# Performance work log

Hardware: AMD Instinct MI355X
Metric: run time of the kernel (lower is better)

## Reference

```python
import jax, jax.numpy as jnp
import numpy as np

SPAN_W = 8      # fixed span width (tokens per span)
HID = 150       # Score hidden dim (hardcoded in source)


def _score_mlp(x, w1, b1, w2, b2, w3, b3):
    # Linear->ReLU->(Dropout=id)->Linear->ReLU->(Dropout=id)->Linear ; out dim 1
    h = jax.nn.relu(x @ w1 + b1)
    h = jax.nn.relu(h @ w2 + b2)
    return h @ w3 + b3


def _make_mlp_params(key, in_dim):
    ks = jax.random.split(key, 6)
    s1 = 1.0 / np.sqrt(in_dim)
    s2 = 1.0 / np.sqrt(HID)
    return (
        jax.random.uniform(ks[0], (in_dim, HID), jnp.float32, -s1, s1),
        jax.random.uniform(ks[1], (HID,), jnp.float32, -s1, s1),
        jax.random.uniform(ks[2], (HID, HID), jnp.float32, -s2, s2),
        jax.random.uniform(ks[3], (HID,), jnp.float32, -s2, s2),
        jax.random.uniform(ks[4], (HID, 1), jnp.float32, -s2, s2),
        jax.random.uniform(ks[5], (1,), jnp.float32, -s2, s2),
    )


def setup_inputs() -> dict:
    key = jax.random.key(0)
    k_emb, k_sp, k_a, k_m, k_p = jax.random.split(key, 5)
    E = 768
    B, T, S = 2, 2048, 96
    encoded_docs = jax.random.normal(k_emb, (B, T, E), jnp.float32)
    span_starts = jnp.sort(
        jax.random.randint(k_sp, (B, S), 0, 2040, dtype=jnp.int64), axis=-1)
    aw1, ab1, aw2, ab2, aw3, ab3 = _make_mlp_params(k_a, E)          # attn Score
    mw1, mb1, mw2, mb2, mw3, mb3 = _make_mlp_params(k_m, 3 * E)      # mention Score
    pw1, pb1, pw2, pb2, pw3, pb3 = _make_mlp_params(k_p, 9 * E)      # pair Score
    return {
        "encoded_docs": encoded_docs, "span_starts": span_starts,
        "aw1": aw1, "ab1": ab1, "aw2": aw2, "ab2": ab2, "aw3": aw3, "ab3": ab3,
        "mw1": mw1, "mb1": mb1, "mw2": mw2, "mb2": mb2, "mw3": mw3, "mb3": mb3,
        "pw1": pw1, "pb1": pb1, "pw2": pw2, "pb2": pb2, "pw3": pw3, "pb3": pb3,
    }


def reference(encoded_docs, span_starts,
              aw1, ab1, aw2, ab2, aw3, ab3,
              mw1, mb1, mw2, mb2, mw3, mb3,
              pw1, pb1, pw2, pb2, pw3, pb3):
    B, T, E = encoded_docs.shape
    S = span_starts.shape[1]

    # --- MentionScore ---
    attns = _score_mlp(encoded_docs, aw1, ab1, aw2, ab2, aw3, ab3)  # [B,T,1]
    starts = span_starts                                              # [B,S]
    ends = starts + (SPAN_W - 1)
    g_start = jnp.take_along_axis(encoded_docs, starts[:, :, None], axis=1)  # [B,S,E]
    g_end = jnp.take_along_axis(encoded_docs, ends[:, :, None], axis=1)      # [B,S,E]
    tok_idx = starts[:, :, None] + jnp.arange(SPAN_W, dtype=starts.dtype)     # [B,S,W]
    flat = tok_idx.reshape(B, S * SPAN_W)
    span_emb = jnp.take_along_axis(encoded_docs, flat[:, :, None], axis=1).reshape(B, S, SPAN_W, E)
    span_attn = jnp.take_along_axis(attns, flat[:, :, None], axis=1).reshape(B, S, SPAN_W, 1)
    g_attn = jnp.sum(span_emb * span_attn, axis=2)                    # [B,S,E]
    g_i = jnp.concatenate([g_start, g_end, g_attn], axis=-1)          # [B,S,3E]
    mention_scores = _score_mlp(g_i, mw1, mb1, mw2, mb2, mw3, mb3)    # [B,S,1]

    # --- PairwiseScore: all pairs (i=span_1, j=span_2) ---
    gi = jnp.broadcast_to(g_i[:, :, None, :], (B, S, S, 3 * E))
    gj = jnp.broadcast_to(g_i[:, None, :, :], (B, S, S, 3 * E))
    pair = jnp.concatenate([gi, gj, gi * gj], axis=-1)                # [B,S,S,9E]
    pair_scores = _score_mlp(pair, pw1, pb1, pw2, pb2, pw3, pb3)      # [B,S,S,1]
    ext = (mention_scores[:, :, None, :] + mention_scores[:, None, :, :] + pair_scores) / 3.0
    return jnp.clip(ext, 0.0, 1.0)
```

## Files before the change

### kernel.cpp

```cpp
#include <hip/hip_runtime.h>

#define EDIM   768
#define E3     2304
#define HIDD   150
#define TT     2048
#define SS     96
#define BB     2

typedef unsigned short u16;
using frag   = __attribute__((ext_vector_type(8))) short;
using f32x4v = __attribute__((ext_vector_type(4))) float;
using u16x8  = __attribute__((ext_vector_type(8))) unsigned short;

__device__ __forceinline__ u16 bf16rn(float f) {
    union { float f; unsigned u; } v; v.f = f;
    unsigned r = v.u + 0x7FFF + ((v.u >> 16) & 1);
    return (u16)(r >> 16);
}
__device__ __forceinline__ float bf16tof(u16 h) {
    union { unsigned u; float f; } v; v.u = ((unsigned)h) << 16;
    return v.f;
}
__device__ __forceinline__ void split2(float f, u16& hi, u16& lo) {
    hi = bf16rn(f); lo = bf16rn(f - bf16tof(hi));
}
__device__ __forceinline__ int swzoff(int row, int qd) {
    return row * 32 + (((qd + (row >> 1)) & 3) << 3);
}
__device__ __forceinline__ void async16(const void* g, void* l) {
    __builtin_amdgcn_global_load_lds(
        (const __attribute__((address_space(1))) void*)g,
        (__attribute__((address_space(3))) void*)l, 16, 0, 0);
}

__global__ __launch_bounds__(256) void k_prep_all(
    const float* __restrict__ pw1, const float* __restrict__ mw1,
    const float* __restrict__ aw1, const float* __restrict__ aw2,
    const float* __restrict__ pw2,
    u16* __restrict__ W12t_hi, u16* __restrict__ W12t_lo,
    u16* __restrict__ AW1t_hi, u16* __restrict__ AW1t_lo,
    u16* __restrict__ AW2t_hi, u16* __restrict__ AW2t_lo,
    u16* __restrict__ PW2t_hi, u16* __restrict__ PW2t_lo)
{
    __shared__ float tile[64][33];
    const int bi = blockIdx.x;
    const int t  = threadIdx.x;

    if (bi < 720) {
        const int k0 = (bi % 36) * 64;
        const int n0 = (bi / 36) * 32;
        const int seg = n0 / 160;
        const int nloc0 = n0 - seg * 160;
        for (int idx = t; idx < 2048; idx += 256) {
            const int kk = idx >> 5, nn = idx & 31;
            const int nl = nloc0 + nn;
            const int k  = k0 + kk;
            float v = 0.f;
            if (nl < HIDD) {
                if (seg == 0)      v = pw1[(long)k * HIDD + nl];
                else if (seg == 1) v = pw1[(long)(E3 + k) * HIDD + nl];
                else if (seg == 2) v = mw1[(long)k * HIDD + nl];
                else               v = pw1[(long)(2 * E3 + k) * HIDD + nl];
            }
            tile[kk][nn] = v;
        }
        __syncthreads();
        for (int idx = t; idx < 2048; idx += 256) {
            const int nn = idx >> 6, kk = idx & 63;
            u16 hi, lo; split2(tile[kk][nn], hi, lo);
            W12t_hi[(long)(n0 + nn) * E3 + k0 + kk] = hi;
            W12t_lo[(long)(n0 + nn) * E3 + k0 + kk] = lo;
        }
    } else if (bi < 1488) {
        const int k = bi - 720;
        if (t < 160) {
            float v = (t < HIDD) ? aw1[k * HIDD + t] : 0.f;
            u16 hi, lo; split2(v, hi, lo);
            AW1t_hi[(long)t * EDIM + k] = hi;
            AW1t_lo[(long)t * EDIM + k] = lo;
        }
    } else {
        const int r = bi - 1488;
        const int k = r % 160;
        const int which = r / 160;
        const float* src = which ? pw2 : aw2;
        u16* dh = which ? PW2t_hi : AW2t_hi;
        u16* dl = which ? PW2t_lo : AW2t_lo;
        if (t < 160) {
            float v = (t < HIDD && k < HIDD) ? src[k * HIDD + t] : 0.f;
            u16 hi, lo; split2(v, hi, lo);
            dh[t * 160 + k] = hi;
            dl[t * 160 + k] = lo;
        }
    }
}

__global__ __launch_bounds__(256) void k_attn1(
    const float* __restrict__ X, const int* __restrict__ spans,
    const u16* __restrict__ AW1t_hi, const u16* __restrict__ AW1t_lo,
    float* __restrict__ AH1)
{
    __shared__ __align__(16) u16 As_hi[32 * 40];
    __shared__ __align__(16) u16 As_lo[32 * 40];
    __shared__ __align__(16) u16 Bs_hi[160 * 40];
    __shared__ __align__(16) u16 Bs_lo[160 * 40];

    const int t    = threadIdx.x;
    const int lane = t & 63;
    const int m    = lane & 15;
    const int quad = lane >> 4;
    const int w    = t >> 6;
    const int mt   = (w & 1) * 16;
    const int nb   = (w >> 1) * 80;
    const int ks   = blockIdx.y;

    const int rr = t >> 3, q = t & 7;
    const int grow = blockIdx.x * 32 + rr;
    const int bs = grow >> 3, sw = grow & 7;
    const int b  = bs / SS;
    const int tok = spans[bs] + sw;
    const float* arow = X + ((long)b * TT + tok) * EDIM;

    f32x4v acc[5];
    #pragma unroll
    for (int ht = 0; ht < 5; ++ht)
        #pragma unroll
        for (int r = 0; r < 4; ++r) acc[ht][r] = 0.f;

    for (int tt = 0; tt < 6; ++tt) {
        const int kk0 = ks * 192 + tt * 32;
        {
            const float4 xv = *(const float4*)&arow[kk0 + q * 4];
            ushort4 hv, lv;
            split2(xv.x, hv.x, lv.x); split2(xv.y, hv.y, lv.y);
            split2(xv.z, hv.z, lv.z); split2(xv.w, hv.w, lv.w);
            *(ushort4*)&As_hi[rr * 40 + q * 4] = hv;
            *(ushort4*)&As_lo[rr * 40 + q * 4] = lv;
        }
        #pragma unroll
        for (int it = 0; it < 3; ++it) {
            const int v = t + it * 256;
            if (v < 640) {
                const int h = v >> 2, qq = v & 3;
                *(uint4*)&Bs_hi[h * 40 + qq * 8] = *(const uint4*)&AW1t_hi[(long)h * EDIM + kk0 + qq * 8];
                *(uint4*)&Bs_lo[h * 40 + qq * 8] = *(const uint4*)&AW1t_lo[(long)h * EDIM + kk0 + qq * 8];
            }
        }
        __syncthreads();
        const frag ah = *(const frag*)&As_hi[(mt + m) * 40 + quad * 8];
        const frag al = *(const frag*)&As_lo[(mt + m) * 40 + quad * 8];
        #pragma unroll
        for (int ht = 0; ht < 5; ++ht) {
            const frag bh = *(const frag*)&Bs_hi[(nb + ht * 16 + m) * 40 + quad * 8];
            const frag bl = *(const frag*)&Bs_lo[(nb + ht * 16 + m) * 40 + quad * 8];
            acc[ht] = __builtin_amdgcn_mfma_f32_16x16x32_bf16(al, bh, acc[ht], 0, 0, 0);
            acc[ht] = __builtin_amdgcn_mfma_f32_16x16x32_bf16(ah, bl, acc[ht], 0, 0, 0);
            acc[ht] = __builtin_amdgcn_mfma_f32_16x16x32_bf16(ah, bh, acc[ht], 0, 0, 0);
        }
        __syncthreads();
    }
    #pragma unroll
    for (int ht = 0; ht < 5; ++ht) {
        #pragma unroll
        for (int r = 0; r < 4; ++r) {
            const int row = blockIdx.x * 32 + mt + quad * 4 + r;
            const int col = nb + ht * 16 + m;
            if (col < HIDD) atomicAdd(&AH1[row * 160 + col], acc[ht][r]);
        }
    }
}

__global__ __launch_bounds__(256) void k_attn2(
    const float* __restrict__ AH1,
    const u16* __restrict__ AW2t_hi, const u16* __restrict__ AW2t_lo,
    const float* __restrict__ ab1, const float* __restrict__ ab2,
    const float* __restrict__ aw3, const float* __restrict__ ab3,
    float* __restrict__ attn_g)
{
    __shared__ __align__(16) u16 As_hi[32 * 40];
    __shared__ __align__(16) u16 As_lo[32 * 40];
    __shared__ __align__(16) u16 Bs_hi[160 * 40];
    __shared__ __align__(16) u16 Bs_lo[160 * 40];
    __shared__ float h1s[32 * 160];
    __shared__ float red[32];

    const int t    = threadIdx.x;
    const int lane = t & 63;
    const int m    = lane & 15;
    const int quad = lane >> 4;
    const int w    = t >> 6;
    const int mt   = (w & 1) * 16;
    const int nb   = (w >> 1) * 80;

    for (int u = t; u < 1280; u += 256) {
        const int row = u / 40, c4 = u - (u / 40) * 40;
        const int c0 = c4 * 4;
        const float4 v = *(const float4*)&AH1[(blockIdx.x * 32 + row) * 160 + c0];
        h1s[row * 160 + c0 + 0] = (c0 + 0 < HIDD) ? fmaxf(v.x + ab1[c0 + 0], 0.f) : 0.f;
        h1s[row * 160 + c0 + 1] = (c0 + 1 < HIDD) ? fmaxf(v.y + ab1[c0 + 1], 0.f) : 0.f;
        h1s[row * 160 + c0 + 2] = (c0 + 2 < HIDD) ? fmaxf(v.z + ab1[c0 + 2], 0.f) : 0.f;
        h1s[row * 160 + c0 + 3] = (c0 + 3 < HIDD) ? fmaxf(v.w + ab1[c0 + 3], 0.f) : 0.f;
    }
    if (t < 32) red[t] = 0.f;
    __syncthreads();

    const int rr = t >> 3, q = t & 7;
    f32x4v acc2[5];
    #pragma unroll
    for (int ht = 0; ht < 5; ++ht)
        #pragma unroll
        for (int r = 0; r < 4; ++r) acc2[ht][r] = 0.f;

    for (int kk = 0; kk < 5; ++kk) {
        {
            const float4 xv = *(const float4*)&h1s[rr * 160 + kk * 32 + q * 4];
            ushort4 hv, lv;
            split2(xv.x, hv.x, lv.x); split2(xv.y, hv.y, lv.y);
            split2(xv.z, hv.z, lv.z); split2(xv.w, hv.w, lv.w);
            *(ushort4*)&As_hi[rr * 40 + q * 4] = hv;
            *(ushort4*)&As_lo[rr * 40 + q * 4] = lv;
        }
        #pragma unroll
        for (int it = 0; it < 3; ++it) {
            const int v = t + it * 256;
            if (v < 640) {
                const int h = v >> 2, qq = v & 3;
                *(uint4*)&Bs_hi[h * 40 + qq * 8] = *(const uint4*)&AW2t_hi[h * 160 + kk * 32 + qq * 8];
                *(uint4*)&Bs_lo[h * 40 + qq * 8] = *(const uint4*)&AW2t_lo[h * 160 + kk * 32 + qq * 8];
            }
        }
        __syncthreads();
        const frag ah = *(const frag*)&As_hi[(mt + m) * 40 + quad * 8];
        const frag al = *(const frag*)&As_lo[(mt + m) * 40 + quad * 8];
        #pragma unroll
        for (int ht = 0; ht < 5; ++ht) {
            const frag bh = *(const frag*)&Bs_hi[(nb + ht * 16 + m) * 40 + quad * 8];
            const frag bl = *(const frag*)&Bs_lo[(nb + ht * 16 + m) * 40 + quad * 8];
            acc2[ht] = __builtin_amdgcn_mfma_f32_16x16x32_bf16(al, bh, acc2[ht], 0, 0, 0);
            acc2[ht] = __builtin_amdgcn_mfma_f32_16x16x32_bf16(ah, bl, acc2[ht], 0, 0, 0);
            acc2[ht] = __builtin_amdgcn_mfma_f32_16x16x32_bf16(ah, bh, acc2[ht], 0, 0, 0);
        }
        __syncthreads();
    }

    float s[4] = {0.f, 0.f, 0.f, 0.f};
    #pragma unroll
    for (int ht = 0; ht < 5; ++ht) {
        const int col = nb + ht * 16 + m;
        if (col < HIDD) {
            const float w3 = aw3[col];
            #pragma unroll
            for (int r = 0; r < 4; ++r)
                s[r] += fmaxf(acc2[ht][r] + ab2[col], 0.f) * w3;
        }
    }
    #pragma unroll
    for (int r = 0; r < 4; ++r) {
        for (int off = 8; off > 0; off >>= 1) s[r] += __shfl_down(s[r], off, 16);
    }
    if (m == 0) {
        #pragma unroll
        for (int r = 0; r < 4; ++r) atomicAdd(&red[mt + quad * 4 + r], s[r]);
    }
    __syncthreads();
    if (t < 32) attn_g[blockIdx.x * 32 + t] = red[t] + ab3[0];
}

__global__ __launch_bounds__(256) void k_span_g(
    const float* __restrict__ X, const int* __restrict__ spans,
    const float* __restrict__ attn_g, float* __restrict__ G_ws,
    u16* __restrict__ Gs_hi, u16* __restrict__ Gs_lo)
{
    __shared__ float a8[8];
    const int t  = threadIdx.x;
    const int bs = blockIdx.x;
    const int b  = bs / SS;
    const int start = spans[bs];
    const float* xb = X + ((long)b * TT + start) * EDIM;
    float* Gp = G_ws + (long)bs * E3;
    u16* Gh = Gs_hi + (long)bs * E3;
    u16* Gl = Gs_lo + (long)bs * E3;
    if (t < 8) a8[t] = attn_g[bs * 8 + t];
    __syncthreads();

    for (int e = t; e < EDIM; e += 256) {
        const float gs = xb[e];
        const float ge = xb[7 * EDIM + e];
        float ga = 0.f;
        #pragma unroll
        for (int w = 0; w < 8; ++w) ga += xb[w * EDIM + e] * a8[w];
        Gp[e] = gs; Gp[EDIM + e] = ge; Gp[2 * EDIM + e] = ga;
        u16 hi, lo;
        split2(gs, hi, lo); Gh[e] = hi;            Gl[e] = lo;
        split2(ge, hi, lo); Gh[EDIM + e] = hi;     Gl[EDIM + e] = lo;
        split2(ga, hi, lo); Gh[2 * EDIM + e] = hi; Gl[2 * EDIM + e] = lo;
    }
}

__global__ __launch_bounds__(256) void k_uvm(
    const u16* __restrict__ Gs_hi, const u16* __restrict__ Gs_lo,
    const u16* __restrict__ W9t_hi, const u16* __restrict__ W9t_lo,
    float* __restrict__ UVM)
{
    __shared__ __align__(16) u16 As_hi[64 * 40];
    __shared__ __align__(16) u16 As_lo[64 * 40];
    __shared__ __align__(16) u16 Bs_hi[160 * 40];
    __shared__ __align__(16) u16 Bs_lo[160 * 40];

    const int t    = threadIdx.x;
    const int mb   = blockIdx.x;
    const int nb   = blockIdx.y;
    const int ks   = blockIdx.z;
    const int lane = t & 63;
    const int m    = lane & 15;
    const int quad = lane >> 4;
    const int w    = t >> 6;
    const int mhalf = (w & 1) * 32;
    const int nbase = (w >> 1) * 80;
    const int arr = t >> 2, aq = t & 3;

    f32x4v acc[2][5];
    #pragma unroll
    for (int i = 0; i < 2; ++i)
        #pragma unroll
        for (int j = 0; j < 5; ++j)
            #pragma unroll
            for (int r = 0; r < 4; ++r) acc[i][j][r] = 0.f;

    for (int tt = 0; tt < 6; ++tt) {
        const int kk0 = ks * 192 + tt * 32;
        *(uint4*)&As_hi[arr * 40 + aq * 8] = *(const uint4*)&Gs_hi[(long)(mb * 64 + arr) * E3 + kk0 + aq * 8];
        *(uint4*)&As_lo[arr * 40 + aq * 8] = *(const uint4*)&Gs_lo[(long)(mb * 64 + arr) * E3 + kk0 + aq * 8];
        #pragma unroll
        for (int it = 0; it < 3; ++it) {
            const int v = t + it * 256;
            if (v < 640) {
                const int h = v >> 2, qq = v & 3;
                *(uint4*)&Bs_hi[h * 40 + qq * 8] = *(const uint4*)&W9t_hi[(long)(nb * 160 + h) * E3 + kk0 + qq * 8];
                *(uint4*)&Bs_lo[h * 40 + qq * 8] = *(const uint4*)&W9t_lo[(long)(nb * 160 + h) * E3 + kk0 + qq * 8];
            }
        }
        __syncthreads();
        frag ah[2], al[2];
        #pragma unroll
        for (int mt = 0; mt < 2; ++mt) {
            ah[mt] = *(const frag*)&As_hi[(mhalf + mt * 16 + m) * 40 + quad * 8];
            al[mt] = *(const frag*)&As_lo[(mhalf + mt * 16 + m) * 40 + quad * 8];
        }
        #pragma unroll
        for (int ht = 0; ht < 5; ++ht) {
            const frag bh = *(const frag*)&Bs_hi[(nbase + ht * 16 + m) * 40 + quad * 8];
            const frag bl = *(const frag*)&Bs_lo[(nbase + ht * 16 + m) * 40 + quad * 8];
            #pragma unroll
            for (int mt = 0; mt < 2; ++mt) {
                acc[mt][ht] = __builtin_amdgcn_mfma_f32_16x16x32_bf16(al[mt], bh, acc[mt][ht], 0, 0, 0);
                acc[mt][ht] = __builtin_amdgcn_mfma_f32_16x16x32_bf16(ah[mt], bl, acc[mt][ht], 0, 0, 0);
                acc[mt][ht] = __builtin_amdgcn_mfma_f32_16x16x32_bf16(ah[mt], bh, acc[mt][ht], 0, 0, 0);
            }
        }
        __syncthreads();
    }
    float* dst = UVM + (long)nb * (192 * 160);
    #pragma unroll
    for (int mt = 0; mt < 2; ++mt) {
        #pragma unroll
        for (int ht = 0; ht < 5; ++ht) {
            #pragma unroll
            for (int r = 0; r < 4; ++r) {
                const int row = mb * 64 + mhalf + mt * 16 + quad * 4 + r;
                const int c   = nbase + ht * 16 + m;
                atomicAdd(&dst[row * 160 + c], acc[mt][ht][r]);
            }
        }
    }
}

__global__ __launch_bounds__(256) void k_mention(
    const float* __restrict__ M_ws,
    const float* __restrict__ mb1,
    const float* __restrict__ mw2, const float* __restrict__ mb2,
    const float* __restrict__ mw3, const float* __restrict__ mb3,
    float* __restrict__ m_ws)
{
    __shared__ float h1m[152];
    __shared__ float h2m[152];
    __shared__ float red[256];
    const int t  = threadIdx.x;
    const int bs = blockIdx.x;
    if (t < HIDD) h1m[t] = fmaxf(M_ws[bs * 160 + t] + mb1[t], 0.f);
    __syncthreads();
    if (t < HIDD) {
        float a = mb2[t];
        for (int k = 0; k < HIDD; ++k) a += h1m[k] * mw2[k * HIDD + t];
        h2m[t] = fmaxf(a, 0.f);
    }
    __syncthreads();
    red[t] = (t < HIDD) ? h2m[t] * mw3[t] : 0.f;
    __syncthreads();
    for (int off = 128; off > 0; off >>= 1) {
        if (t < off) red[t] += red[t + off];
        __syncthreads();
    }
    if (t == 0) m_ws[bs] = red[0] + mb3[0];
}

__global__ __launch_bounds__(256) void k_pairmm(
    const float* __restrict__ G_ws,
    const u16* __restrict__ PCt_hi, const u16* __restrict__ PCt_lo,
    float* __restrict__ H1parts)
{
    __shared__ float gis[768];
    __shared__ __align__(16) float gjst[96 * 32];
    __shared__ __align__(16) u16 As_hi[96 * 32];
    __shared__ __align__(16) u16 As_lo[96 * 32];
    __shared__ __align__(16) u16 Bs_hi[160 * 32];
    __shared__ __align__(16) u16 Bs_lo[160 * 32];

    const int t  = threadIdx.x;
    const int ks = blockIdx.x;
    const int i  = blockIdx.y;
    const int b  = blockIdx.z;
    const int ksbase = ks * 768;
    const int jt0 = i >> 4;
    const int ntiles = 6 - jt0;
    const int j0 = jt0 * 16;
    const int R  = 96 - j0;
    const int nI = R >> 3;

    const int lane = t & 63;
    const int m    = lane & 15;
    const int quad = lane >> 4;
    const int w    = t >> 6;
    const int hb   = (w & 1) * 80;
    const int apar = w >> 1;

    const int Bl_h  = lane >> 2;
    const int Bl_c  = lane & 3;
    const int gj_r  = lane >> 3;
    const int gj_c  = lane & 7;

    const float* Gi = G_ws + (long)(b * SS + i) * E3 + ksbase;
    for (int e = t; e < 768; e += 256) gis[e] = Gi[e];

    f32x4v acc[3][5];
    #pragma unroll
    for (int jt = 0; jt < 3; ++jt)
        #pragma unroll
        for (int ht = 0; ht < 5; ++ht)
            #pragma unroll
            for (int r = 0; r < 4; ++r) acc[jt][ht][r] = 0.f;

    for (int tt = 0; tt < 24; ++tt) {
        const int kk0 = ksbase + tt * 32;
        for (int q2 = w; q2 < 10; q2 += 4) {
            const int h  = q2 * 16 + Bl_h;
            const int qd = (Bl_c - (h >> 1)) & 3;
            const long so = (long)h * E3 + kk0 + qd * 8;
            async16(&PCt_hi[so], &Bs_hi[q2 * 512]);
            async16(&PCt_lo[so], &Bs_lo[q2 * 512]);
        }
        for (int g2 = w; g2 < nI; g2 += 4) {
            const int row = j0 + g2 * 8 + gj_r;
            async16(&G_ws[(long)(b * SS + row) * E3 + kk0 + gj_c * 4],
                    &gjst[g2 * 256]);
        }
        __syncthreads();

        for (int u = t; u < R * 4; u += 256) {
            const int rr = u >> 2, qd = u & 3;
            const float4 g0 = *(const float4*)&gjst[rr * 32 + qd * 8];
            const float4 g1 = *(const float4*)&gjst[rr * 32 + qd * 8 + 4];
            const int kl = tt * 32 + qd * 8;
            u16x8 hv, lv; u16 h, l;
            split2(g0.x * gis[kl + 0], h, l); hv[0] = h; lv[0] = l;
            split2(g0.y * gis[kl + 1], h, l); hv[1] = h; lv[1] = l;
            split2(g0.z * gis[kl + 2], h, l); hv[2] = h; lv[2] = l;
            split2(g0.w * gis[kl + 3], h, l); hv[3] = h; lv[3] = l;
            split2(g1.x * gis[kl + 4], h, l); hv[4] = h; lv[4] = l;
            split2(g1.y * gis[kl + 5], h, l); hv[5] = h; lv[5] = l;
            split2(g1.z * gis[kl + 6], h, l); hv[6] = h; lv[6] = l;
            split2(g1.w * gis[kl + 7], h, l); hv[7] = h; lv[7] = l;
            const int o = swzoff(rr, qd);
            *(u16x8*)&As_hi[o] = hv;
            *(u16x8*)&As_lo[o] = lv;
        }
        __syncthreads();

        frag ah[3], al[3];
        #pragma unroll
        for (int u = 0; u < 3; ++u) {
            const int a = apar + 2 * u;
            if (a < ntiles) {
                const int o = swzoff(a * 16 + m, quad);
                ah[u] = *(const frag*)&As_hi[o];
                al[u] = *(const frag*)&As_lo[o];
            }
        }
        #pragma unroll
        for (int ht = 0; ht < 5; ++ht) {
            const int o = swzoff(hb + ht * 16 + m, quad);
            const frag bh = *(const frag*)&Bs_hi[o];
            const frag bl = *(const frag*)&Bs_lo[o];
            #pragma unroll
            for (int u = 0; u < 3; ++u) {
                if (apar + 2 * u < ntiles) {
                    acc[u][ht] = __builtin_amdgcn_mfma_f32_16x16x32_bf16(al[u], bh, acc[u][ht], 0, 0, 0);
                    acc[u][ht] = __builtin_amdgcn_mfma_f32_16x16x32_bf16(ah[u], bl, acc[u][ht], 0, 0, 0);
                    acc[u][ht] = __builtin_amdgcn_mfma_f32_16x16x32_bf16(ah[u], bh, acc[u][ht], 0, 0, 0);
                }
            }
        }
        __syncthreads();
    }

    float* dst = H1parts + (long)ks * ((long)BB * SS * SS * 160);
    #pragma unroll
    for (int u = 0; u < 3; ++u) {
        const int a = apar + 2 * u;
        if (a < ntiles) {
            #pragma unroll
            for (int ht = 0; ht < 5; ++ht) {
                #pragma unroll
                for (int r = 0; r < 4; ++r) {
                    const int j = (jt0 + a) * 16 + quad * 4 + r;
                    const int h = hb + ht * 16 + m;
                    dst[((long)(b * SS + i) * SS + j) * 160 + h] = acc[u][ht][r];
                }
            }
        }
    }
}

__global__ __launch_bounds__(256) void k_pair2(
    const float* __restrict__ H1a, const float* __restrict__ H1b,
    const float* __restrict__ H1c,
    const float* __restrict__ U_ws, const float* __restrict__ V_ws,
    const float* __restrict__ pb1, const float* __restrict__ m_ws,
    const u16* __restrict__ PW2t_hi, const u16* __restrict__ PW2t_lo,
    const float* __restrict__ pb2, const float* __restrict__ pw3,
    const float* __restrict__ pb3,
    float* __restrict__ out)
{
    __shared__ __align__(16) u16 As_hi[96 * 168];
    __shared__ __align__(16) u16 As_lo[96 * 168];
    __shared__ __align__(16) u16 Bs_hi[160 * 40];
    __shared__ __align__(16) u16 Bs_lo[160 * 40];
    __shared__ float uv[160];
    __shared__ float red[96];

    const int t  = threadIdx.x;
    const int bi = blockIdx.x;
    const int b  = bi / SS;
    const int ii = bi - b * SS;

    if (t < 160) uv[t] = U_ws[bi * 160 + t] + ((t < HIDD) ? pb1[t] : 0.f);
    if (t < 96) red[t] = 0.f;
    __syncthreads();

    for (int u = t; u < 96 * 40; u += 256) {
        const int j = u / 40, hq = u - (u / 40) * 40;
        const int h0 = hq * 4;
        const int mn = ii < j ? ii : j;
        const int mx = ii < j ? j : ii;
        const long idx = (((long)b * SS + mn) * SS + mx) * 160 + h0;
        const float4 a  = *(const float4*)&H1a[idx];
        const float4 bb = *(const float4*)&H1b[idx];
        const float4 c  = *(const float4*)&H1c[idx];
        const float4 vv = *(const float4*)&V_ws[(b * SS + j) * 160 + h0];
        const float p0 = fmaxf(a.x + bb.x + c.x + vv.x + uv[h0 + 0], 0.f);
        const float p1 = fmaxf(a.y + bb.y + c.y + vv.y + uv[h0 + 1], 0.f);
        const float p2 = fmaxf(a.z + bb.z + c.z + vv.z + uv[h0 + 2], 0.f);
        const float p3 = fmaxf(a.w + bb.w + c.w + vv.w + uv[h0 + 3], 0.f);
        ushort4 hv, lv;
        split2(p0, hv.x, lv.x); split2(p1, hv.y, lv.y);
        split2(p2, hv.z, lv.z); split2(p3, hv.w, lv.w);
        *(ushort4*)&As_hi[j * 168 + h0] = hv;
        *(ushort4*)&As_lo[j * 168 + h0] = lv;
    }
    __syncthreads();

    const int lane = t & 63;
    const int m    = lane & 15;
    const int quad = lane >> 4;
    const int w    = t >> 6;
    const int jbs  = (w & 1) * 48;
    const int nbs  = (w >> 1) * 80;

    f32x4v acc[3][5];
    #pragma unroll
    for (int jt = 0; jt < 3; ++jt)
        #pragma unroll
        for (int ht = 0; ht < 5; ++ht)
            #pragma unroll
            for (int r = 0; r < 4; ++r) acc[jt][ht][r] = 0.f;

    for (int kk = 0; kk < 5; ++kk) {
        #pragma unroll
        for (int it = 0; it < 3; ++it) {
            const int v = t + it * 256;
            if (v < 640) {
                const int n = v >> 2, qq = v & 3;
                *(uint4*)&Bs_hi[n * 40 + qq * 8] = *(const uint4*)&PW2t_hi[n * 160 + kk * 32 + qq * 8];
                *(uint4*)&Bs_lo[n * 40 + qq * 8] = *(const uint4*)&PW2t_lo[n * 160 + kk * 32 + qq * 8];
            }
        }
        __syncthreads();
        frag ah[3], al[3];
        #pragma unroll
        for (int jt = 0; jt < 3; ++jt) {
            ah[jt] = *(const frag*)&As_hi[(jbs + jt * 16 + m) * 168 + kk * 32 + quad * 8];
            al[jt] = *(const frag*)&As_lo[(jbs + jt * 16 + m) * 168 + kk * 32 + quad * 8];
        }
        #pragma unroll
        for (int ht = 0; ht < 5; ++ht) {
            const frag bh = *(const frag*)&Bs_hi[(nbs + ht * 16 + m) * 40 + quad * 8];
            const frag bl = *(const frag*)&Bs_lo[(nbs + ht * 16 + m) * 40 + quad * 8];
            #pragma unroll
            for (int jt = 0; jt < 3; ++jt) {
                acc[jt][ht] = __builtin_amdgcn_mfma_f32_16x16x32_bf16(al[jt], bh, acc[jt][ht], 0, 0, 0);
                acc[jt][ht] = __builtin_amdgcn_mfma_f32_16x16x32_bf16(ah[jt], bl, acc[jt][ht], 0, 0, 0);
                acc[jt][ht] = __builtin_amdgcn_mfma_f32_16x16x32_bf16(ah[jt], bh, acc[jt][ht], 0, 0, 0);
            }
        }
        __syncthreads();
    }

    float s[3][4];
    #pragma unroll
    for (int jt = 0; jt < 3; ++jt)
        #pragma unroll
        for (int r = 0; r < 4; ++r) s[jt][r] = 0.f;
    #pragma unroll
    for (int ht = 0; ht < 5; ++ht) {
        const int col = nbs + ht * 16 + m;
        if (col < HIDD) {
            const float w3 = pw3[col];
            const float b2 = pb2[col];
            #pragma unroll
            for (int jt = 0; jt < 3; ++jt)
                #pragma unroll
                for (int r = 0; r < 4; ++r)
                    s[jt][r] += fmaxf(acc[jt][ht][r] + b2, 0.f) * w3;
        }
    }
    #pragma unroll
    for (int jt = 0; jt < 3; ++jt)
        #pragma unroll
        for (int r = 0; r < 4; ++r)
            for (int off = 8; off > 0; off >>= 1)
                s[jt][r] += __shfl_down(s[jt][r], off, 16);
    if (m == 0) {
        #pragma unroll
        for (int jt = 0; jt < 3; ++jt)
            #pragma unroll
            for (int r = 0; r < 4; ++r)
                atomicAdd(&red[jbs + jt * 16 + quad * 4 + r], s[jt][r]);
    }
    __syncthreads();

    if (t < 96) {
        const float sc = red[t] + pb3[0];
        const float v = (m_ws[bi] + m_ws[b * SS + t] + sc) * (1.f / 3.f);
        out[(long)bi * SS + t] = fminf(fmaxf(v, 0.f), 1.f);
    }
}

extern "C" void kernel_launch(void* const* d_in, const int* in_sizes, int n_in,
                              void* d_out, int out_size, void* d_ws, size_t ws_size,
                              hipStream_t stream)
{
    const float* X     = (const float*)d_in[0];
    const int*   spans = (const int*)  d_in[1];
    const float* aw1 = (const float*)d_in[2];
    const float* ab1 = (const float*)d_in[3];
    const float* aw2 = (const float*)d_in[4];
    const float* ab2 = (const float*)d_in[5];
    const float* aw3 = (const float*)d_in[6];
    const float* ab3 = (const float*)d_in[7];
    const float* mw1 = (const float*)d_in[8];
    const float* mb1 = (const float*)d_in[9];
    const float* mw2 = (const float*)d_in[10];
    const float* mb2 = (const float*)d_in[11];
    const float* mw3 = (const float*)d_in[12];
    const float* mb3 = (const float*)d_in[13];
    const float* pw1 = (const float*)d_in[14];
    const float* pb1 = (const float*)d_in[15];
    const float* pw2 = (const float*)d_in[16];
    const float* pb2 = (const float*)d_in[17];
    const float* pw3 = (const float*)d_in[18];
    const float* pb3 = (const float*)d_in[19];
    float* out = (float*)d_out;

    char* p = (char*)d_ws;
    float* attn_g  = (float*)p;  p += 6144;
    float* G_ws    = (float*)p;  p += (long)442368 * 4;
    u16*   Gs_hi   = (u16*)p;    p += (long)442368 * 2;
    u16*   Gs_lo   = (u16*)p;    p += (long)442368 * 2;
    float* UVM     = (float*)p;  p += (long)3 * 192 * 160 * 4;
    float* AH1     = (float*)p;  p += (long)1536 * 160 * 4;
    float* m_ws    = (float*)p;  p += 1024;
    u16*   W12t_hi = (u16*)p;    p += (long)640 * E3 * 2;
    u16*   W12t_lo = (u16*)p;    p += (long)640 * E3 * 2;
    u16*   AW1t_hi = (u16*)p;    p += (long)160 * EDIM * 2;
    u16*   AW1t_lo = (u16*)p;    p += (long)160 * EDIM * 2;
    u16*   AW2t_hi = (u16*)p;    p += 160 * 160 * 2;
    u16*   AW2t_lo = (u16*)p;    p += 160 * 160 * 2;
    u16*   PW2t_hi = (u16*)p;    p += 160 * 160 * 2;
    u16*   PW2t_lo = (u16*)p;    p += 160 * 160 * 2;
    float* H1parts = (float*)p;

    float* U_ws = UVM;
    float* V_ws = UVM + 192 * 160;
    float* M_ws = UVM + 2 * 192 * 160;
    const u16* PCt_hi = W12t_hi + (long)480 * E3;
    const u16* PCt_lo = W12t_lo + (long)480 * E3;

    hipMemsetAsync(UVM, 0, ((size_t)3 * 192 * 160 + (size_t)1536 * 160) * sizeof(float), stream);

    k_prep_all<<<dim3(1808), 256, 0, stream>>>(pw1, mw1, aw1, aw2, pw2,
                                               W12t_hi, W12t_lo, AW1t_hi, AW1t_lo,
                                               AW2t_hi, AW2t_lo, PW2t_hi, PW2t_lo);

    k_attn1<<<dim3(48, 4), 256, 0, stream>>>(X, spans, AW1t_hi, AW1t_lo, AH1);
    k_attn2<<<dim3(48), 256, 0, stream>>>(AH1, AW2t_hi, AW2t_lo, ab1, ab2, aw3, ab3, attn_g);
    k_span_g<<<dim3(BB * SS), 256, 0, stream>>>(X, spans, attn_g, G_ws, Gs_hi, Gs_lo);
    k_uvm<<<dim3(3, 3, 12), 256, 0, stream>>>(Gs_hi, Gs_lo, W12t_hi, W12t_lo, UVM);
    k_mention<<<dim3(BB * SS), 256, 0, stream>>>(M_ws, mb1, mw2, mb2, mw3, mb3, m_ws);
    k_pairmm<<<dim3(3, SS, BB), 256, 0, stream>>>(G_ws, PCt_hi, PCt_lo, H1parts);

    const long H1sz = (long)BB * SS * SS * 160;
    k_pair2<<<dim3(BB * SS), 256, 0, stream>>>(
        H1parts, H1parts + H1sz, H1parts + 2 * H1sz,
        U_ws, V_ws, pb1, m_ws, PW2t_hi, PW2t_lo, pb2, pw3, pb3, out);
}
```

Measured before the change: 225.6 us.

## Double-buffer async LDS loads in pair matmul and trim barriers

```diff
diff --git a/kernel.cpp b/kernel.cpp
--- a/kernel.cpp
+++ b/kernel.cpp
@@ -31,6 +31,10 @@
     __builtin_amdgcn_global_load_lds(
         (const __attribute__((address_space(1))) void*)g,
         (__attribute__((address_space(3))) void*)l, 16, 0, 0);
+}
+__device__ __forceinline__ void barrier_lds_only() {
+    __builtin_amdgcn_s_waitcnt(0xC07F);
+    __builtin_amdgcn_s_barrier();
 }
 
 __global__ __launch_bounds__(256) void k_prep_all(
@@ -410,11 +414,11 @@
     float* __restrict__ H1parts)
 {
     __shared__ float gis[768];
-    __shared__ __align__(16) float gjst[96 * 32];
+    __shared__ __align__(16) float gjst[2][96 * 32];
     __shared__ __align__(16) u16 As_hi[96 * 32];
     __shared__ __align__(16) u16 As_lo[96 * 32];
-    __shared__ __align__(16) u16 Bs_hi[160 * 32];
-    __shared__ __align__(16) u16 Bs_lo[160 * 32];
+    __shared__ __align__(16) u16 Bs_hi[2][160 * 32];
+    __shared__ __align__(16) u16 Bs_lo[2][160 * 32];
 
     const int t  = threadIdx.x;
     const int ks = blockIdx.x;
@@ -439,37 +443,43 @@
     const int gj_r  = lane >> 3;
     const int gj_c  = lane & 7;
 
-    const float* Gi = G_ws + (long)(b * SS + i) * E3 + ksbase;
-    for (int e = t; e < 768; e += 256) gis[e] = Gi[e];
-
-    f32x4v acc[3][5];
-    #pragma unroll
-    for (int jt = 0; jt < 3; ++jt)
-        #pragma unroll
-        for (int ht = 0; ht < 5; ++ht)
-            #pragma unroll
-            for (int r = 0; r < 4; ++r) acc[jt][ht][r] = 0.f;
-
-    for (int tt = 0; tt < 24; ++tt) {
+    auto issue = [&](int tt, int buf) {
         const int kk0 = ksbase + tt * 32;
         for (int q2 = w; q2 < 10; q2 += 4) {
             const int h  = q2 * 16 + Bl_h;
             const int qd = (Bl_c - (h >> 1)) & 3;
             const long so = (long)h * E3 + kk0 + qd * 8;
-            async16(&PCt_hi[so], &Bs_hi[q2 * 512]);
-            async16(&PCt_lo[so], &Bs_lo[q2 * 512]);
+            async16(&PCt_hi[so], &Bs_hi[buf][q2 * 512]);
+            async16(&PCt_lo[so], &Bs_lo[buf][q2 * 512]);
         }
         for (int g2 = w; g2 < nI; g2 += 4) {
             const int row = j0 + g2 * 8 + gj_r;
             async16(&G_ws[(long)(b * SS + row) * E3 + kk0 + gj_c * 4],
-                    &gjst[g2 * 256]);
-        }
-        __syncthreads();
+                    &gjst[buf][g2 * 256]);
+        }
+    };
+
+    const float* Gi = G_ws + (long)(b * SS + i) * E3 + ksbase;
+    for (int e = t; e < 768; e += 256) gis[e] = Gi[e];
+    issue(0, 0);
+
+    f32x4v acc[3][5];
+    #pragma unroll
+    for (int jt = 0; jt < 3; ++jt)
+        #pragma unroll
+        for (int ht = 0; ht < 5; ++ht)
+            #pragma unroll
+            for (int r = 0; r < 4; ++r) acc[jt][ht][r] = 0.f;
+
+    for (int tt = 0; tt < 24; ++tt) {
+        const int cur = tt & 1;
+        __syncthreads();
+        if (tt < 23) issue(tt + 1, cur ^ 1);
 
         for (int u = t; u < R * 4; u += 256) {
             const int rr = u >> 2, qd = u & 3;
-            const float4 g0 = *(const float4*)&gjst[rr * 32 + qd * 8];
-            const float4 g1 = *(const float4*)&gjst[rr * 32 + qd * 8 + 4];
+            const float4 g0 = *(const float4*)&gjst[cur][rr * 32 + qd * 8];
+            const float4 g1 = *(const float4*)&gjst[cur][rr * 32 + qd * 8 + 4];
             const int kl = tt * 32 + qd * 8;
             u16x8 hv, lv; u16 h, l;
             split2(g0.x * gis[kl + 0], h, l); hv[0] = h; lv[0] = l;
@@ -484,7 +494,7 @@
             *(u16x8*)&As_hi[o] = hv;
             *(u16x8*)&As_lo[o] = lv;
         }
-        __syncthreads();
+        barrier_lds_only();
 
         frag ah[3], al[3];
         #pragma unroll
@@ -499,8 +509,8 @@
         #pragma unroll
         for (int ht = 0; ht < 5; ++ht) {
             const int o = swzoff(hb + ht * 16 + m, quad);
-            const frag bh = *(const frag*)&Bs_hi[o];
-            const frag bl = *(const frag*)&Bs_lo[o];
+            const frag bh = *(const frag*)&Bs_hi[cur][o];
+            const frag bl = *(const frag*)&Bs_lo[cur][o];
             #pragma unroll
             for (int u = 0; u < 3; ++u) {
                 if (apar + 2 * u < ntiles) {
@@ -510,7 +520,6 @@
                 }
             }
         }
-        __syncthreads();
     }
 
     float* dst = H1parts + (long)ks * ((long)BB * SS * SS * 160);
```

Result: slower. 232.5 us (+3.1%).
